# Kernel tuning notes

Measured on AMD Instinct MI355X. Metric: run time of the kernel, lower is better.

Reference implementation:

```python
import jax, jax.numpy as jnp
import numpy as np

B, C, H, W = 8, 256, 64, 64
HID = C // 2


def setup_inputs() -> dict:
    key = jax.random.key(0)
    k = jax.random.split(key, 5)
    s = 0.05
    return {
        "x": jax.random.normal(k[0], (B, C, H, W), jnp.float32),
        "w_phi": jax.random.normal(k[1], (HID, C), jnp.float32) * s,
        "w_theta": jax.random.normal(k[2], (HID, C), jnp.float32) * s,
        "w_g": jax.random.normal(k[3], (HID, C), jnp.float32) * s,
        "w_out": jax.random.normal(k[4], (C, HID), jnp.float32) * s,
    }


def reference(x, w_phi, w_theta, w_g, w_out):
    b, c, h, w = x.shape
    n = h * w
    hid = w_phi.shape[0]
    xf = x.reshape(b, c, n)                              # [B, C, N]
    phi = jnp.einsum('oc,bcn->bon', w_phi, xf)           # [B, hid, N]
    theta = jnp.einsum('oc,bcn->bno', w_theta, xf)       # [B, N, hid]
    g = jnp.einsum('oc,bcn->bno', w_g, xf)               # [B, N, hid]
    # Faithful to torch: pw /= d**(-0.5)  == multiply by sqrt(d)
    scale = jnp.asarray(hid, x.dtype) ** 0.5
    pw = jnp.einsum('bno,bom->bnm', theta, phi) * scale  # [B, N, N]
    pw = jax.nn.softmax(pw, axis=-1)
    y = jnp.einsum('bnm,bmo->bno', pw, g)                # [B, N, hid]
    y = y.transpose(0, 2, 1).reshape(b, hid, h, w)
    out = x + jnp.einsum('co,bohw->bchw', w_out, y)
    return out
```

## Files before the change

kernel.cpp:

```cpp
#include <hip/hip_runtime.h>

typedef __attribute__((ext_vector_type(8))) short bf16x8;
typedef __attribute__((ext_vector_type(8))) _Float16 f16x8;
typedef __attribute__((ext_vector_type(4))) float f32x4;
typedef __attribute__((ext_vector_type(16))) float f32x16;
typedef __attribute__((ext_vector_type(8))) unsigned short u16x8;

#define MFMA16(a, b, c)  __builtin_amdgcn_mfma_f32_16x16x32_bf16((a), (b), (c), 0, 0, 0)
#define MFMA16F(a, b, c) __builtin_amdgcn_mfma_f32_16x16x32_f16((a), (b), (c), 0, 0, 0)
#define MFMA32(a, b, c)  __builtin_amdgcn_mfma_f32_32x32x16_bf16((a), (b), (c), 0, 0, 0)
#define MFMA32F(a, b, c) __builtin_amdgcn_mfma_f32_32x32x16_f16((a), (b), (c), 0, 0, 0)

__device__ __forceinline__ unsigned short f2bf(float v) {
    unsigned u = __float_as_uint(v);
    return (unsigned short)((u + 0x7fffu + ((u >> 16) & 1u)) >> 16);
}
__device__ __forceinline__ float bf2f(unsigned short h) {
    return __uint_as_float(((unsigned)h) << 16);
}
__device__ __forceinline__ unsigned short f2h(float v) {
    union { _Float16 h; unsigned short u; } cv; cv.h = (_Float16)v; return cv.u;
}
__device__ __forceinline__ void gll16(const void* g, void* l) {
    __builtin_amdgcn_global_load_lds(
        (const __attribute__((address_space(1))) unsigned int*)g,
        (__attribute__((address_space(3))) unsigned int*)l, 16, 0, 0);
}
__device__ __forceinline__ unsigned cvtpk(float lo, float hi) {
    unsigned r;
    asm("v_cvt_pk_bf16_f32 %0, %1, %2" : "=v"(r) : "v"(lo), "v"(hi));
    return r;
}
#define PSWAP(a, b) asm volatile("v_permlane32_swap_b32 %0, %1" : "+v"(a), "+v"(b))

__device__ __forceinline__ f32x16 zero16() {
    f32x16 z;
#pragma unroll
    for (int j = 0; j < 16; j++) z[j] = 0.f;
    return z;
}

#define NB 8
#define NC 256
#define NN 4096
#define HID 128
#define ELEMS (NB * NN * HID)

__global__ __launch_bounds__(256, 2)
void proj_kernel(const float* __restrict__ x,
                 const float* __restrict__ w_theta,
                 const float* __restrict__ w_phi,
                 const float* __restrict__ w_g,
                 unsigned short* __restrict__ Qf, unsigned short* __restrict__ Kf,
                 unsigned short* __restrict__ Vt) {
    __shared__ __align__(16) unsigned char LdsRaw[128 * 65 * 4];
    float (*xs)[129] = reinterpret_cast<float(*)[129]>(LdsRaw);
    unsigned int (*Tb)[65] = reinterpret_cast<unsigned int(*)[65]>(LdsRaw);

    const int t = threadIdx.x;
    const int w = t >> 6, lane = t & 63;
    const int g = lane >> 4, c = lane & 15;
    const int n0 = blockIdx.x * 128;
    const int which = blockIdx.y;
    const int b = blockIdx.z;
    const float* wsel = (which == 0) ? w_theta : ((which == 1) ? w_phi : w_g);

    f32x4 acc[2][8];
#pragma unroll
    for (int mi = 0; mi < 2; mi++)
#pragma unroll
        for (int nt = 0; nt < 8; nt++) acc[mi][nt] = (f32x4){0.f, 0.f, 0.f, 0.f};

    const int srow = w * 16 + (lane >> 2);
    const int snq = (lane & 3) * 32;

    for (int k0 = 0; k0 < NC; k0 += 64) {
        __syncthreads();
        {
            const float* src = x + ((size_t)(b * NC + k0 + srow)) * NN + n0 + snq;
            float4 v[8];
#pragma unroll
            for (int u = 0; u < 8; u++) v[u] = *(const float4*)(src + 4 * u);
#pragma unroll
            for (int u = 0; u < 8; u++) {
                xs[srow][snq + 4 * u + 0] = v[u].x;
                xs[srow][snq + 4 * u + 1] = v[u].y;
                xs[srow][snq + 4 * u + 2] = v[u].z;
                xs[srow][snq + 4 * u + 3] = v[u].w;
            }
        }
        __syncthreads();

        if (which < 2) {
#pragma unroll
            for (int s = 0; s < 2; s++) {
                f16x8 wf2[2];
#pragma unroll
                for (int mi = 0; mi < 2; mi++) {
                    const float* wp = wsel + (size_t)(w * 32 + mi * 16 + c) * NC + k0 + s * 32 + g * 8;
                    float av[8];
                    *(float4*)&av[0] = *(const float4*)wp;
                    *(float4*)&av[4] = *(const float4*)(wp + 4);
#pragma unroll
                    for (int j = 0; j < 8; j++) wf2[mi][j] = (_Float16)av[j];
                }
#pragma unroll
                for (int nt = 0; nt < 8; nt++) {
                    f16x8 xf;
#pragma unroll
                    for (int j = 0; j < 8; j++) xf[j] = (_Float16)xs[s * 32 + g * 8 + j][nt * 16 + c];
#pragma unroll
                    for (int mi = 0; mi < 2; mi++)
                        acc[mi][nt] = MFMA16F(wf2[mi], xf, acc[mi][nt]);
                }
            }
        } else {
#pragma unroll
            for (int s = 0; s < 2; s++) {
                bf16x8 wh[2];
#pragma unroll
                for (int mi = 0; mi < 2; mi++) {
                    const float* wp = wsel + (size_t)(w * 32 + mi * 16 + c) * NC + k0 + s * 32 + g * 8;
                    float av[8];
                    *(float4*)&av[0] = *(const float4*)wp;
                    *(float4*)&av[4] = *(const float4*)(wp + 4);
#pragma unroll
                    for (int j = 0; j < 8; j++) wh[mi][j] = (short)f2bf(av[j]);
                }
#pragma unroll
                for (int nt = 0; nt < 8; nt++) {
                    bf16x8 xh;
#pragma unroll
                    for (int j = 0; j < 8; j++) xh[j] = (short)f2bf(xs[s * 32 + g * 8 + j][nt * 16 + c]);
#pragma unroll
                    for (int mi = 0; mi < 2; mi++)
                        acc[mi][nt] = MFMA16(wh[mi], xh, acc[mi][nt]);
                }
            }
        }
    }

    if (which == 2) {
#pragma unroll
        for (int mi = 0; mi < 2; mi++)
#pragma unroll
            for (int nt = 0; nt < 8; nt++)
#pragma unroll
                for (int r = 0; r < 4; r++) {
                    int o = w * 32 + mi * 16 + 4 * g + r;
                    Vt[((size_t)(b * HID + o)) * NN + n0 + nt * 16 + c] = f2bf(acc[mi][nt][r]);
                }
    } else {
        unsigned short* dh = (which == 0) ? Qf : Kf;
        const float qscale = (which == 0) ? 16.32223142f : 1.0f;
        for (int h = 0; h < 2; h++) {
            __syncthreads();
#pragma unroll
            for (int mi = 0; mi < 2; mi++)
#pragma unroll
                for (int q2 = 0; q2 < 4; q2++) {
                    int nt = h * 4 + q2;
#pragma unroll
                    for (int r = 0; r < 4; r++)
                        Tb[w * 32 + mi * 16 + 4 * g + r][q2 * 16 + c] =
                            (unsigned)f2h(acc[mi][nt][r] * qscale);
                }
            __syncthreads();
            {
                int nl = t & 63;
                int og = (t >> 6) * 32;
                int n = n0 + h * 64 + nl;
                u16x8 vh[4];
#pragma unroll
                for (int k = 0; k < 32; k++)
                    vh[k >> 3][k & 7] = (unsigned short)Tb[og + k][nl];
                size_t base = ((size_t)(b * NN + n)) * HID + og;
#pragma unroll
                for (int q = 0; q < 4; q++)
                    *(u16x8*)(dh + base + q * 8) = vh[q];
            }
        }
    }
}

template<int ZBITS>
__global__ __launch_bounds__(256, 3)
void attn_kernel(const unsigned short* __restrict__ Qf, const unsigned short* __restrict__ Kf,
                 const unsigned short* __restrict__ Vt,
                 unsigned short* __restrict__ Yp, float* __restrict__ Ms, float* __restrict__ Ss,
                 int kv_len) {
    __shared__ __align__(16) unsigned char KV_lds[2][16384];

    const int t = threadIdx.x;
    const int w = t >> 6, lane = t & 63;
    const int l31 = lane & 31, hi = lane >> 5;
    const int bid = blockIdx.x;
    const int b = bid & 7;
    const int z = (bid >> 3) & ((1 << ZBITS) - 1);
    const int qx = bid >> (3 + ZBITS);
    const int q0 = qx * 128 + w * 32;

    const int kvb = z * kv_len;
    const char* KG = (const char*)(Kf + ((size_t)(b * NN) + kvb) * HID);
    const char* VG = (const char*)(Vt + ((size_t)(b * HID)) * NN + kvb);

    const int si0 = w * 2, si1 = w * 2 + 1;
    const int krow0 = si0 * 4 + (lane >> 4), krow1 = si1 * 4 + (lane >> 4);
    const int kq = lane & 15;
    const int kqg0 = kq ^ (krow0 & 15), kqg1 = kq ^ (krow1 & 15);
    const int vrow0 = si0 * 16 + (lane >> 2), vrow1 = si1 * 16 + (lane >> 2);
    const int vm = lane & 3;
    const int vmg0 = vm ^ ((vrow0 >> 1) & 3), vmg1 = vm ^ ((vrow1 >> 1) & 3);

#define STAGE(buf, kvoff)                                                                        \
    do {                                                                                         \
        gll16(KG + (size_t)((kvoff) + krow0) * 256 + kqg0 * 16, (buf) + si0 * 1024);             \
        gll16(KG + (size_t)((kvoff) + krow1) * 256 + kqg1 * 16, (buf) + si1 * 1024);             \
        gll16(VG + (size_t)vrow0 * 8192 + (size_t)(kvoff) * 2 + vmg0 * 16, (buf) + 8192 + si0 * 1024); \
        gll16(VG + (size_t)vrow1 * 8192 + (size_t)(kvoff) * 2 + vmg1 * 16, (buf) + 8192 + si1 * 1024); \
    } while (0)

    STAGE(&KV_lds[0][0], 0);

    f16x8 qf[8];
    {
        const unsigned short* qp = Qf + ((size_t)(b * NN) + q0 + l31) * HID + hi * 8;
#pragma unroll
        for (int s = 0; s < 8; s++) qf[s] = *(const f16x8*)(qp + s * 16);
    }

    float mstar = -3.0e38f, sacc = 0.f;
    f32x16 yacc[4];
#pragma unroll
    for (int dt = 0; dt < 4; dt++) yacc[dt] = zero16();

    const int ntl = kv_len >> 5;
    int cur = 0;
    const int krbase = l31 * 256;
    const int kkey = l31 & 15;
    const int vkey = (l31 >> 1) & 3;

    for (int tI = 0; tI < ntl; ++tI) {
        if (tI + 1 < ntl) {
            STAGE(&KV_lds[cur ^ 1][0], (tI + 1) * 32);
            asm volatile("s_waitcnt vmcnt(4)" ::: "memory");
        } else {
            asm volatile("s_waitcnt vmcnt(0)" ::: "memory");
        }
        __builtin_amdgcn_sched_barrier(0);
        __builtin_amdgcn_s_barrier();

        const unsigned char* K_l = &KV_lds[cur][0];
        const unsigned char* V_l = &KV_lds[cur][8192];

        f32x16 stv = zero16();
        __builtin_amdgcn_s_setprio(1);
#pragma unroll
        for (int s = 0; s < 8; s++) {
            const int off = krbase + (((2 * s + hi) ^ kkey) * 16);
            f16x8 kf = *(const f16x8*)(K_l + off);
            stv = MFMA32F(kf, qf[s], stv);
        }
        __builtin_amdgcn_s_setprio(0);

        float m = stv[0];
#pragma unroll
        for (int r = 1; r < 16; r++) m = fmaxf(m, stv[r]);
        m = fmaxf(m, __shfl_xor(m, 32));

        if (__any(m > mstar + 65.f)) {
            float nm = fmaxf(mstar, m);
            float corr = exp2f(mstar - nm);
            mstar = nm;
            sacc *= corr;
            float cr[16];
#pragma unroll
            for (int r = 0; r < 16; r++)
                cr[r] = __shfl(corr, (r & 3) + 8 * (r >> 2) + 4 * hi);
#pragma unroll
            for (int dt = 0; dt < 4; dt++)
#pragma unroll
                for (int r = 0; r < 16; r++) yacc[dt][r] *= cr[r];
        }

        float p[16];
#pragma unroll
        for (int r = 0; r < 16; r++) p[r] = exp2f(stv[r] - mstar);
        float ls = 0.f;
#pragma unroll
        for (int r = 0; r < 16; r++) ls += p[r];
        sacc += ls;

        unsigned X0 = cvtpk(p[0], p[1]),   X1 = cvtpk(p[2], p[3]);
        unsigned X2 = cvtpk(p[4], p[5]),   X3 = cvtpk(p[6], p[7]);
        unsigned X4 = cvtpk(p[8], p[9]),   X5 = cvtpk(p[10], p[11]);
        unsigned X6 = cvtpk(p[12], p[13]), X7 = cvtpk(p[14], p[15]);
        PSWAP(X0, X2); PSWAP(X1, X3);
        PSWAP(X4, X6); PSWAP(X5, X7);
        union { unsigned u[4]; bf16x8 v; } pa, pb;
        pa.u[0] = X0; pa.u[1] = X1; pa.u[2] = X2; pa.u[3] = X3;
        pb.u[0] = X4; pb.u[1] = X5; pb.u[2] = X6; pb.u[3] = X7;
        bf16x8 pf0 = pa.v, pf1 = pb.v;

        __builtin_amdgcn_s_setprio(1);
#pragma unroll
        for (int dt = 0; dt < 4; dt++) {
            const int vbase = (dt * 32 + l31) * 64;
            bf16x8 v0 = *(const bf16x8*)(V_l + vbase + ((hi ^ vkey) * 16));
            bf16x8 v1 = *(const bf16x8*)(V_l + vbase + (((2 + hi) ^ vkey) * 16));
            yacc[dt] = MFMA32(pf0, v0, yacc[dt]);
            yacc[dt] = MFMA32(pf1, v1, yacc[dt]);
        }
        __builtin_amdgcn_s_setprio(0);

        __builtin_amdgcn_sched_barrier(0);
        __builtin_amdgcn_s_barrier();
        cur ^= 1;
    }

    float stot = sacc + __shfl_xor(sacc, 32);

    if (ZBITS == 0) {
        float inv = 1.0f / stot;
        float ivr[16];
#pragma unroll
        for (int r = 0; r < 16; r++)
            ivr[r] = __shfl(inv, (r & 3) + 8 * (r >> 2) + 4 * hi);
        const size_t obase = (size_t)(b * NN) + q0;
#pragma unroll
        for (int dt = 0; dt < 4; dt++)
#pragma unroll
            for (int r = 0; r < 16; r++) {
                int q = (r & 3) + 8 * (r >> 2) + 4 * hi;
                Yp[(obase + q) * HID + dt * 32 + l31] = f2bf(yacc[dt][r] * ivr[r]);
            }
    } else {
        const size_t base = (((size_t)z * NB + b) * NN + q0);
#pragma unroll
        for (int dt = 0; dt < 4; dt++)
#pragma unroll
            for (int r = 0; r < 16; r++) {
                int q = (r & 3) + 8 * (r >> 2) + 4 * hi;
                Yp[(base + q) * HID + dt * 32 + l31] = f2bf(yacc[dt][r]);
            }
        if (hi == 0) {
            Ms[base + l31] = mstar;
            Ss[base + l31] = stot;
        }
    }
#undef STAGE
}

template<int NS>
__global__ __launch_bounds__(256, 2)
void out_kernel(const float* __restrict__ x, const float* __restrict__ w_out,
                const unsigned short* __restrict__ Yp,
                const float* __restrict__ Ms, const float* __restrict__ Ss,
                float* __restrict__ out) {
    __shared__ __align__(16) unsigned short Yl[128][136];

    const int t = threadIdx.x;
    const int w = t >> 6, lane = t & 63;
    const int g = lane >> 4, c = lane & 15;
    const int n0 = blockIdx.x * 128;
    const int b = blockIdx.y;

    {
        int nl = t >> 1, oh = (t & 1) * 64;
        size_t qi = (size_t)b * NN + n0 + nl;
        if (NS == 0) {
            const unsigned short* src = Yp + qi * HID + oh;
#pragma unroll
            for (int i = 0; i < 8; i++)
                *(u16x8*)&Yl[nl][oh + i * 8] = *(const u16x8*)(src + i * 8);
        } else {
            const size_t NBNN = (size_t)NB * NN;
            float Mv[NS > 0 ? NS : 1], Wt[NS > 0 ? NS : 1];
            float M = -3.0e38f;
#pragma unroll
            for (int zz = 0; zz < NS; zz++) { Mv[zz] = Ms[zz * NBNN + qi]; M = fmaxf(M, Mv[zz]); }
            float S = 0.f;
#pragma unroll
            for (int zz = 0; zz < NS; zz++) { Wt[zz] = exp2f(Mv[zz] - M); S += Ss[zz * NBNN + qi] * Wt[zz]; }
            float invS = 1.f / S;
#pragma unroll
            for (int zz = 0; zz < NS; zz++) Wt[zz] *= invS;
#pragma unroll
            for (int i = 0; i < 8; i++) {
                float f[8] = {0.f, 0.f, 0.f, 0.f, 0.f, 0.f, 0.f, 0.f};
#pragma unroll
                for (int zz = 0; zz < NS; zz++) {
                    u16x8 a = *(const u16x8*)(Yp + (zz * NBNN + qi) * HID + oh + i * 8);
#pragma unroll
                    for (int j = 0; j < 8; j++) f[j] = fmaf(bf2f(a[j]), Wt[zz], f[j]);
                }
                u16x8 vv;
#pragma unroll
                for (int j = 0; j < 8; j++) vv[j] = f2bf(f[j]);
                *(u16x8*)&Yl[nl][oh + i * 8] = vv;
            }
        }
    }
    __syncthreads();

    f32x4 acc[4][8];
#pragma unroll
    for (int mi = 0; mi < 4; mi++)
#pragma unroll
        for (int nt = 0; nt < 8; nt++) acc[mi][nt] = (f32x4){0.f, 0.f, 0.f, 0.f};

#pragma unroll
    for (int s = 0; s < 4; s++) {
        bf16x8 wf[4];
#pragma unroll
        for (int mi = 0; mi < 4; mi++) {
            const float* wp = w_out + (size_t)(w * 64 + mi * 16 + c) * HID + s * 32 + g * 8;
            float av[8];
            *(float4*)&av[0] = *(const float4*)wp;
            *(float4*)&av[4] = *(const float4*)(wp + 4);
#pragma unroll
            for (int j = 0; j < 8; j++) wf[mi][j] = (short)f2bf(av[j]);
        }
#pragma unroll
        for (int nt = 0; nt < 8; nt++) {
            bf16x8 yf = *(const bf16x8*)&Yl[nt * 16 + c][s * 32 + g * 8];
#pragma unroll
            for (int mi = 0; mi < 4; mi++) acc[mi][nt] = MFMA16(wf[mi], yf, acc[mi][nt]);
        }
    }

#pragma unroll
    for (int mi = 0; mi < 4; mi++)
#pragma unroll
        for (int nt = 0; nt < 8; nt++)
#pragma unroll
            for (int r = 0; r < 4; r++) {
                int cg = w * 64 + mi * 16 + 4 * g + r;
                size_t idx = ((size_t)(b * NC + cg)) * NN + n0 + nt * 16 + c;
                out[idx] = x[idx] + acc[mi][nt][r];
            }
}

extern "C" void kernel_launch(void* const* d_in, const int* in_sizes, int n_in,
                              void* d_out, int out_size, void* d_ws, size_t ws_size,
                              hipStream_t stream) {
    const float* x = (const float*)d_in[0];
    const float* w_phi = (const float*)d_in[1];
    const float* w_theta = (const float*)d_in[2];
    const float* w_g = (const float*)d_in[3];
    const float* w_out = (const float*)d_in[4];
    float* out = (float*)d_out;

    const size_t BUF = (size_t)ELEMS * 2;
    const size_t MSB = (size_t)NB * NN * 4;
    if (ws_size < 4 * BUF) return;

    unsigned short* Qf = (unsigned short*)d_ws;
    unsigned short* Kf = (unsigned short*)((char*)d_ws + 1 * BUF);
    unsigned short* Vt = (unsigned short*)((char*)d_ws + 2 * BUF);

    proj_kernel<<<dim3(32, 3, 8), 256, 0, stream>>>(x, w_theta, w_phi, w_g, Qf, Kf, Vt);

    if (ws_size >= 7 * BUF + 8 * MSB) {
        unsigned short* Yp = (unsigned short*)((char*)d_ws + 3 * BUF);
        float* Ms = (float*)((char*)d_ws + 7 * BUF);
        float* Ss = (float*)((char*)d_ws + 7 * BUF + 4 * MSB);
        attn_kernel<2><<<dim3(1024), 256, 0, stream>>>(Qf, Kf, Vt, Yp, Ms, Ss, NN / 4);
        out_kernel<4><<<dim3(32, NB), 256, 0, stream>>>(x, w_out, Yp, Ms, Ss, out);
    } else if (ws_size >= 5 * BUF + 4 * MSB) {
        unsigned short* Yp = (unsigned short*)((char*)d_ws + 3 * BUF);
        float* Ms = (float*)((char*)d_ws + 5 * BUF);
        float* Ss = (float*)((char*)d_ws + 5 * BUF + 2 * MSB);
        attn_kernel<1><<<dim3(512), 256, 0, stream>>>(Qf, Kf, Vt, Yp, Ms, Ss, NN / 2);
        out_kernel<2><<<dim3(32, NB), 256, 0, stream>>>(x, w_out, Yp, Ms, Ss, out);
    } else {
        unsigned short* Yb = (unsigned short*)((char*)d_ws + 3 * BUF);
        attn_kernel<0><<<dim3(256), 256, 0, stream>>>(Qf, Kf, Vt, Yb, nullptr, nullptr, NN);
        out_kernel<0><<<dim3(32, NB), 256, 0, stream>>>(x, w_out, Yb, nullptr, nullptr, out);
    }
}
```

Measured before the change: 168.5 us.

## Software-pipeline QK^T one tile ahead with 4-stage K/V LDS ring

Grows the K/V LDS buffer from a double buffer to a four-slot ring with loads issued three tiles ahead. The QK^T MFMAs for the next tile now run before the softmax of the current tile, so matrix work overlaps the exp/max VALU work. One barrier per iteration is removed. In exchange the kernel uses 64KB of LDS, and launch bounds drop to 2 blocks per CU, which lowers occupancy and raises register pressure because two score tiles are live at once.

```diff
diff --git a/kernel.cpp b/kernel.cpp
--- a/kernel.cpp
+++ b/kernel.cpp
@@ -184,12 +184,12 @@
 }
 
 template<int ZBITS>
-__global__ __launch_bounds__(256, 3)
+__global__ __launch_bounds__(256, 2)
 void attn_kernel(const unsigned short* __restrict__ Qf, const unsigned short* __restrict__ Kf,
                  const unsigned short* __restrict__ Vt,
                  unsigned short* __restrict__ Yp, float* __restrict__ Ms, float* __restrict__ Ss,
                  int kv_len) {
-    __shared__ __align__(16) unsigned char KV_lds[2][16384];
+    __shared__ __align__(16) unsigned char KV_lds[4][16384];
 
     const int t = threadIdx.x;
     const int w = t >> 6, lane = t & 63;
@@ -220,7 +220,27 @@
         gll16(VG + (size_t)vrow1 * 8192 + (size_t)(kvoff) * 2 + vmg1 * 16, (buf) + 8192 + si1 * 1024); \
     } while (0)
 
+    const int krbase = l31 * 256;
+    const int kkey = l31 & 15;
+    const int vkey = (l31 >> 1) & 3;
+
+#define QKT(dst, kptr)                                                        \
+    do {                                                                      \
+        (dst) = zero16();                                                     \
+        __builtin_amdgcn_s_setprio(1);                                        \
+        _Pragma("unroll")                                                     \
+        for (int s = 0; s < 8; s++) {                                         \
+            const int off = krbase + (((2 * s + hi) ^ kkey) * 16);            \
+            f16x8 kf = *(const f16x8*)((kptr) + off);                         \
+            (dst) = MFMA32F(kf, qf[s], (dst));                                \
+        }                                                                     \
+        __builtin_amdgcn_s_setprio(0);                                        \
+    } while (0)
+
+    const int ntl = kv_len >> 5;
+
     STAGE(&KV_lds[0][0], 0);
+    if (ntl > 1) STAGE(&KV_lds[1][0], 32);
 
     f16x8 qf[8];
     {
@@ -234,35 +254,29 @@
 #pragma unroll
     for (int dt = 0; dt < 4; dt++) yacc[dt] = zero16();
 
-    const int ntl = kv_len >> 5;
-    int cur = 0;
-    const int krbase = l31 * 256;
-    const int kkey = l31 & 15;
-    const int vkey = (l31 >> 1) & 3;
+    if (ntl > 1) { asm volatile("s_waitcnt vmcnt(4)" ::: "memory"); }
+    else         { asm volatile("s_waitcnt vmcnt(0)" ::: "memory"); }
+    __builtin_amdgcn_sched_barrier(0);
+    __builtin_amdgcn_s_barrier();
+    __builtin_amdgcn_sched_barrier(0);
+    if (ntl > 2) STAGE(&KV_lds[2][0], 64);
+    f32x16 stv_prev;
+    QKT(stv_prev, &KV_lds[0][0]);
 
     for (int tI = 0; tI < ntl; ++tI) {
-        if (tI + 1 < ntl) {
-            STAGE(&KV_lds[cur ^ 1][0], (tI + 1) * 32);
-            asm volatile("s_waitcnt vmcnt(4)" ::: "memory");
-        } else {
-            asm volatile("s_waitcnt vmcnt(0)" ::: "memory");
-        }
+        if (tI + 2 < ntl) { asm volatile("s_waitcnt vmcnt(4)" ::: "memory"); }
+        else              { asm volatile("s_waitcnt vmcnt(0)" ::: "memory"); }
         __builtin_amdgcn_sched_barrier(0);
         __builtin_amdgcn_s_barrier();
-
-        const unsigned char* K_l = &KV_lds[cur][0];
-        const unsigned char* V_l = &KV_lds[cur][8192];
-
-        f32x16 stv = zero16();
-        __builtin_amdgcn_s_setprio(1);
-#pragma unroll
-        for (int s = 0; s < 8; s++) {
-            const int off = krbase + (((2 * s + hi) ^ kkey) * 16);
-            f16x8 kf = *(const f16x8*)(K_l + off);
-            stv = MFMA32F(kf, qf[s], stv);
-        }
-        __builtin_amdgcn_s_setprio(0);
-
+        __builtin_amdgcn_sched_barrier(0);
+
+        if (tI + 3 < ntl) STAGE(&KV_lds[(tI + 3) & 3][0], (tI + 3) * 32);
+
+        f32x16 stv_next;
+        const bool have_next = (tI + 1 < ntl);
+        if (have_next) QKT(stv_next, &KV_lds[(tI + 1) & 3][0]);
+
+        f32x16 stv = stv_prev;
         float m = stv[0];
 #pragma unroll
         for (int r = 1; r < 16; r++) m = fmaxf(m, stv[r]);
@@ -302,6 +316,7 @@
         pb.u[0] = X4; pb.u[1] = X5; pb.u[2] = X6; pb.u[3] = X7;
         bf16x8 pf0 = pa.v, pf1 = pb.v;
 
+        const unsigned char* V_l = &KV_lds[tI & 3][8192];
         __builtin_amdgcn_s_setprio(1);
 #pragma unroll
         for (int dt = 0; dt < 4; dt++) {
@@ -313,9 +328,7 @@
         }
         __builtin_amdgcn_s_setprio(0);
 
-        __builtin_amdgcn_sched_barrier(0);
-        __builtin_amdgcn_s_barrier();
-        cur ^= 1;
+        if (have_next) stv_prev = stv_next;
     }
 
     float stot = sacc + __shfl_xor(sacc, 32);
@@ -348,6 +361,7 @@
             Ss[base + l31] = stot;
         }
     }
+#undef QKT
 #undef STAGE
 }
 
```

New measurement: 176.9 us. 1.05x slower.
